# Kernel tuning notes

Hardware: AMD Instinct MI355X
Metric: run time of the kernel (lower is better)

## Reference

```python
import jax, jax.numpy as jnp
import numpy as np

BS, NQ, DIM, HEADS, POINTS, LEVELS = 2, 4096, 768, 6, 4, 1
HD = DIM // HEADS
H = W = 64
NV = H * W
EPS = 1e-6


def setup_inputs() -> dict:
    key = jax.random.key(0)
    ks = jax.random.split(key, 16)
    s = 0.02  # param init scale
    return {
        "query": jax.random.normal(ks[0], (BS, NQ, DIM), jnp.float32),
        "reference_points": jax.random.uniform(ks[1], (BS, NQ, LEVELS, 2), jnp.float32),
        "feat": jax.random.normal(ks[2], (BS, NV, DIM), jnp.float32),
        "spatial_shapes": np.array([[H, W]], dtype=np.int64),
        "level_start_index": np.array([0], dtype=np.int64),
        "ln_w": jnp.ones((DIM,), jnp.float32),
        "ln_b": jnp.zeros((DIM,), jnp.float32),
        "vp_w": jax.random.normal(ks[3], (DIM, DIM), jnp.float32) * s,
        "vp_b": jnp.zeros((DIM,), jnp.float32),
        "off_w": jax.random.normal(ks[4], (DIM, HEADS * LEVELS * POINTS * 2), jnp.float32) * s,
        "off_b": jax.random.normal(ks[5], (HEADS * LEVELS * POINTS * 2,), jnp.float32),
        "aw_w": jax.random.normal(ks[6], (DIM, HEADS * LEVELS * POINTS), jnp.float32) * s,
        "aw_b": jnp.zeros((HEADS * LEVELS * POINTS,), jnp.float32),
        "out_w": jax.random.normal(ks[7], (DIM, DIM), jnp.float32) * s,
        "out_b": jnp.zeros((DIM,), jnp.float32),
        "gamma": jax.random.normal(ks[8], (DIM,), jnp.float32) * 0.1,
    }


def _layernorm(x, w, b):
    mu = jnp.mean(x, axis=-1, keepdims=True)
    var = jnp.mean(jnp.square(x - mu), axis=-1, keepdims=True)
    return (x - mu) * jax.lax.rsqrt(var + EPS) * w + b


def _bilinear_sample(img, loc):
    # img: (bs, heads, H, W, hd); loc: (bs, nq, heads, points, 2) in [0,1]
    # matches torch.grid_sample(align_corners=False, padding_mode='zeros')
    bs, heads, h, w, hd = img.shape
    x = loc[..., 0] * w - 0.5
    y = loc[..., 1] * h - 0.5
    x0 = jnp.floor(x)
    y0 = jnp.floor(y)
    wx = x - x0
    wy = y - y0
    x0i = x0.astype(jnp.int32)
    y0i = y0.astype(jnp.int32)
    bi = jnp.arange(bs)[:, None, None, None]
    hi = jnp.arange(heads)[None, None, :, None]

    def gather(yi, xi):
        valid = (xi >= 0) & (xi < w) & (yi >= 0) & (yi < h)
        v = img[bi, hi, jnp.clip(yi, 0, h - 1), jnp.clip(xi, 0, w - 1)]
        return v * valid[..., None].astype(img.dtype)

    v00 = gather(y0i, x0i)
    v01 = gather(y0i, x0i + 1)
    v10 = gather(y0i + 1, x0i)
    v11 = gather(y0i + 1, x0i + 1)
    wx = wx[..., None]
    wy = wy[..., None]
    return (v00 * (1 - wy) * (1 - wx) + v01 * (1 - wy) * wx
            + v10 * wy * (1 - wx) + v11 * wy * wx)


def _msda(q, value, reference_points, spatial_shapes, off_w, off_b, aw_w, aw_b, out_w, out_b):
    bs, nq, _ = q.shape
    nv = value.shape[1]
    value = value.reshape(bs, nv, HEADS, HD)
    offsets = (q @ off_w + off_b).reshape(bs, nq, HEADS, LEVELS, POINTS, 2)
    aw = jax.nn.softmax(q @ aw_w + aw_b, axis=-1).reshape(bs, nq, HEADS, LEVELS, POINTS)
    # offset_normalizer = [W_l, H_l] per level
    norm = jnp.asarray(np.asarray(spatial_shapes)[:, ::-1], jnp.float32)  # (L, 2)
    loc = reference_points[:, :, None, :, None, :] + offsets / norm[None, None, None, :, None, :]
    # loc: (bs, nq, heads, levels, points, 2)
    out = jnp.zeros((bs, nq, HEADS, HD), jnp.float32)
    start = 0
    for l in range(LEVELS):
        h_l, w_l = int(spatial_shapes[l][0]), int(spatial_shapes[l][1])
        img = value[:, start:start + h_l * w_l].reshape(bs, h_l, w_l, HEADS, HD).transpose(0, 3, 1, 2, 4)
        sampled = _bilinear_sample(img, loc[:, :, :, l])  # (bs, nq, heads, points, hd)
        out = out + jnp.einsum('bnhpd,bnhp->bnhd', sampled, aw[:, :, :, l])
        start += h_l * w_l
    return out.reshape(bs, nq, DIM) @ out_w + out_b


def reference(query, reference_points, feat, spatial_shapes, level_start_index,
              ln_w, ln_b, vp_w, vp_b, off_w, off_b, aw_w, aw_b, out_w, out_b, gamma):
    q = _layernorm(query, ln_w, ln_b)
    value = feat @ vp_w + vp_b
    attn = _msda(q, value, reference_points, spatial_shapes,
                 off_w, off_b, aw_w, aw_b, out_w, out_b)
    # identity = zeros, dropout = 0 -> attn as-is; residual scale by gamma
    return query + gamma * attn
```

## Files before the change

### kernel.cpp

```cpp
#include <hip/hip_runtime.h>
#include <hip/hip_bf16.h>
#include <math.h>

#define BSZ 2
#define NQ 4096
#define DIM 768
#define HEADS 6
#define POINTS 4
#define HD 128
#define HW_DIM 64
#define NV (HW_DIM*HW_DIM)
#define M_TOTAL (BSZ*NQ)
#define KDIM 768
#define KSPLIT 2
#define KPART (KDIM/KSPLIT)

#define BM 64
#define BN 128
#define BKK 64
#define NBLK_M (M_TOTAL/BM)
#define NBLK_N (DIM/BN)
#define GEMM_GRID (NBLK_M*NBLK_N)
#define LN_BLOCKS (M_TOTAL/4)
#define TR_BLOCKS (576+576+72)

#define A_TILE (BM*BKK)
#define B_TILE (BN*BKK)
#define SMEM_U16 (2*(A_TILE+B_TILE))

typedef __attribute__((ext_vector_type(8))) short bf16x8;
typedef __attribute__((ext_vector_type(4))) float f32x4;
typedef unsigned int u32;
typedef unsigned short u16;

__device__ inline u16 f2bf(float f) {
    union { float f; u32 u; } v; v.f = f;
    u32 r = v.u + 0x7fffu + ((v.u >> 16) & 1u);
    return (u16)(r >> 16);
}

#define GLD16(g, l) __builtin_amdgcn_global_load_lds( \
    (const __attribute__((address_space(1))) u32*)(g), \
    (__attribute__((address_space(3))) u32*)(l), 16, 0, 0)

__global__ __launch_bounds__(256) void prep_kernel(
        const float* __restrict__ x, const float* __restrict__ lnw,
        const float* __restrict__ lnb, u16* __restrict__ q,
        const float* __restrict__ feat, u16* __restrict__ feat_bf,
        const float* __restrict__ vp_w,  u16* __restrict__ vp_wt,
        const float* __restrict__ out_w, u16* __restrict__ out_wt,
        const float* __restrict__ off_w, const float* __restrict__ aw_w,
        u16* __restrict__ oaw_wt) {
    int b = blockIdx.x;
    if (b < LN_BLOCKS) {
        int wave = threadIdx.x >> 6, lane = threadIdx.x & 63;
        int row = b * 4 + wave;
        int c = lane * 4;
        const float* xr = x + (size_t)row * DIM;
        const float* fr = feat + (size_t)row * DIM;
        float4 v0 = *(const float4*)(xr + c);
        float4 v1 = *(const float4*)(xr + c + 256);
        float4 v2 = *(const float4*)(xr + c + 512);
        float4 f0 = *(const float4*)(fr + c);
        float4 f1 = *(const float4*)(fr + c + 256);
        float4 f2 = *(const float4*)(fr + c + 512);
        u16* fb = feat_bf + (size_t)row * DIM;
        ushort4 fo;
        fo.x = f2bf(f0.x); fo.y = f2bf(f0.y); fo.z = f2bf(f0.z); fo.w = f2bf(f0.w);
        *(ushort4*)(fb + c) = fo;
        fo.x = f2bf(f1.x); fo.y = f2bf(f1.y); fo.z = f2bf(f1.z); fo.w = f2bf(f1.w);
        *(ushort4*)(fb + c + 256) = fo;
        fo.x = f2bf(f2.x); fo.y = f2bf(f2.y); fo.z = f2bf(f2.z); fo.w = f2bf(f2.w);
        *(ushort4*)(fb + c + 512) = fo;

        float s  = v0.x+v0.y+v0.z+v0.w + v1.x+v1.y+v1.z+v1.w + v2.x+v2.y+v2.z+v2.w;
        float ss = v0.x*v0.x+v0.y*v0.y+v0.z*v0.z+v0.w*v0.w
                 + v1.x*v1.x+v1.y*v1.y+v1.z*v1.z+v1.w*v1.w
                 + v2.x*v2.x+v2.y*v2.y+v2.z*v2.z+v2.w*v2.w;
        #pragma unroll
        for (int st = 1; st < 64; st <<= 1) {
            s  += __shfl_xor(s,  st, 64);
            ss += __shfl_xor(ss, st, 64);
        }
        float mean = s * (1.0f / DIM);
        float var  = ss * (1.0f / DIM) - mean * mean;
        float rstd = rsqrtf(var + 1e-6f);
        u16* qr = q + (size_t)row * DIM;
        #pragma unroll
        for (int g = 0; g < 3; g++) {
            float4 v = (g == 0) ? v0 : (g == 1) ? v1 : v2;
            int cc = c + g * 256;
            const float4 ww = *(const float4*)(lnw + cc);
            const float4 bb = *(const float4*)(lnb + cc);
            ushort4 o;
            o.x = f2bf((v.x - mean) * rstd * ww.x + bb.x);
            o.y = f2bf((v.y - mean) * rstd * ww.y + bb.y);
            o.z = f2bf((v.z - mean) * rstd * ww.z + bb.z);
            o.w = f2bf((v.w - mean) * rstd * ww.w + bb.w);
            *(ushort4*)(qr + cc) = o;
        }
    } else {
        int t = b - LN_BLOCKS;
        int z, xk, yk;
        if (t < 576)      { z = 0; xk = t % 24; yk = t / 24; }
        else if (t < 1152){ z = 1; t -= 576; xk = t % 24; yk = t / 24; }
        else              { z = 2; t -= 1152; xk = t % 3; yk = t / 3; }
        __shared__ float tile[32][33];
        int n0 = xk * 32, k0 = yk * 32;
        int tx = threadIdx.x & 31, ty = threadIdx.x >> 5;
        const float* src = (z == 0) ? vp_w : (z == 1) ? out_w : nullptr;
        u16* dst = (z == 0) ? vp_wt : (z == 1) ? out_wt : oaw_wt;
        #pragma unroll
        for (int r = 0; r < 4; r++) {
            int k = k0 + ty + r * 8, n = n0 + tx;
            float v = 0.0f;
            if (z < 2) {
                v = src[(size_t)k * DIM + n];
            } else {
                if (n < 48) v = off_w[(size_t)k * 48 + n];
                else if (n < 72) v = aw_w[(size_t)k * 24 + (n - 48)];
            }
            tile[ty + r * 8][tx] = v;
        }
        __syncthreads();
        #pragma unroll
        for (int r = 0; r < 4; r++) {
            int nn = ty + r * 8, kk = tx;
            int drow = n0 + nn;
            if (z == 2 && drow >= 80) continue;
            dst[(size_t)drow * KDIM + k0 + kk] = f2bf(tile[kk][nn]);
        }
    }
}

__device__ __forceinline__ void gemm_big_body(int b, u16* __restrict__ smem,
        const u16* __restrict__ A, const u16* __restrict__ Bt,
        const float* __restrict__ bias, void* __restrict__ Cout,
        int storeBF16, const float* __restrict__ resid,
        const float* __restrict__ gamma) {
    u16* As = smem;
    u16* Bs = smem + 2 * A_TILE;
    int tid = threadIdx.x, w = tid >> 6, lane = tid & 63;
    int lm = lane & 15, quad = lane >> 4;
    int xcd = b & 7, idx = b >> 3;
    int mb = xcd * 16 + idx / NBLK_N;
    int nb = idx % NBLK_N;
    int m0 = mb * BM, n0 = nb * BN;
    int wr = w & 1, wc = w >> 1;

    int srow = lane >> 3;
    int scol = (lane & 7) ^ srow;
    const u16* Ab = A + (size_t)m0 * KDIM;
    const u16* Bb = Bt + (size_t)n0 * KDIM;

    f32x4 acc[2][4];
    #pragma unroll
    for (int i = 0; i < 2; i++)
        #pragma unroll
        for (int j = 0; j < 4; j++) acc[i][j] = (f32x4){0.f, 0.f, 0.f, 0.f};

    int aoff[2][2], boff[4][2];
    #pragma unroll
    for (int i = 0; i < 2; i++) {
        int row = wr * 32 + i * 16 + lm;
        #pragma unroll
        for (int kk = 0; kk < 2; kk++)
            aoff[i][kk] = row * BKK + (((quad + 4 * kk) ^ (row & 7)) << 3);
    }
    #pragma unroll
    for (int j = 0; j < 4; j++) {
        int row = wc * 64 + j * 16 + lm;
        #pragma unroll
        for (int kk = 0; kk < 2; kk++)
            boff[j][kk] = row * BKK + (((quad + 4 * kk) ^ (row & 7)) << 3);
    }

    auto stage = [&](int buf, int k0) {
        #pragma unroll
        for (int r = 0; r < 2; r++) {
            int row = r * 32 + w * 8 + srow;
            GLD16(Ab + (size_t)row * KDIM + k0 + scol * 8,
                  As + buf * A_TILE + (r * 32 + w * 8) * BKK);
        }
        #pragma unroll
        for (int r = 0; r < 4; r++) {
            int row = r * 32 + w * 8 + srow;
            GLD16(Bb + (size_t)row * KDIM + k0 + scol * 8,
                  Bs + buf * B_TILE + (r * 32 + w * 8) * BKK);
        }
    };

    stage(0, 0);
    __syncthreads();
    const int NT = KDIM / BKK;
    for (int t = 0; t < NT; t++) {
        if (t + 1 < NT) stage((t + 1) & 1, (t + 1) * BKK);
        const u16* Ap = As + (t & 1) * A_TILE;
        const u16* Bp = Bs + (t & 1) * B_TILE;
        #pragma unroll
        for (int kk = 0; kk < 2; kk++) {
            bf16x8 af[2], bf[4];
            #pragma unroll
            for (int i = 0; i < 2; i++) af[i] = *(const bf16x8*)(Ap + aoff[i][kk]);
            #pragma unroll
            for (int j = 0; j < 4; j++) bf[j] = *(const bf16x8*)(Bp + boff[j][kk]);
            #pragma unroll
            for (int i = 0; i < 2; i++)
                #pragma unroll
                for (int j = 0; j < 4; j++)
                    acc[i][j] = __builtin_amdgcn_mfma_f32_16x16x32_bf16(af[i], bf[j], acc[i][j], 0, 0, 0);
        }
        __syncthreads();
    }

    #pragma unroll
    for (int j = 0; j < 4; j++) {
        int col = n0 + wc * 64 + j * 16 + lm;
        float bb = bias[col];
        #pragma unroll
        for (int i = 0; i < 2; i++) {
            #pragma unroll
            for (int r = 0; r < 4; r++) {
                int row = m0 + wr * 32 + i * 16 + quad * 4 + r;
                size_t idxo = (size_t)row * DIM + col;
                float v = acc[i][j][r] + bb;
                if (storeBF16) {
                    ((u16*)Cout)[idxo] = f2bf(v);
                } else {
                    ((float*)Cout)[idxo] = resid[idxo] + gamma[col] * v;
                }
            }
        }
    }
}

#define SA_TILE (64*32)
#define SB_TILE (80*32)
__device__ __forceinline__ void gemm_small_body(int mblk, int part,
        u16* __restrict__ smem,
        const u16* __restrict__ A, const u16* __restrict__ Bt,
        const float* __restrict__ b0, const float* __restrict__ b1,
        float* __restrict__ C) {
    u16* As2 = smem;
    u16* Bs2 = smem + 2 * SA_TILE;
    int tid = threadIdx.x, wave = tid >> 6, lane = tid & 63;
    int lm = lane & 15, quad = lane >> 4;
    int m0 = mblk * 64;
    int kbase = part * KPART;
    f32x4 acc[5];
    #pragma unroll
    for (int i = 0; i < 5; i++) acc[i] = (f32x4){0.f, 0.f, 0.f, 0.f};
    int lrow = lane >> 2, lcol = (lane & 3) * 8;

    auto stage = [&](int buf, int k0) {
        for (int c = wave; c < 9; c += 4) {
            if (c < 4) {
                GLD16(A + (size_t)(m0 + c * 16 + lrow) * KDIM + k0 + lcol,
                      As2 + buf * SA_TILE + c * 16 * 32);
            } else {
                GLD16(Bt + (size_t)((c - 4) * 16 + lrow) * KDIM + k0 + lcol,
                      Bs2 + buf * SB_TILE + (c - 4) * 16 * 32);
            }
        }
    };

    stage(0, kbase);
    __syncthreads();
    const int NT = KPART / 32;
    for (int t = 0; t < NT; t++) {
        if (t + 1 < NT) stage((t + 1) & 1, kbase + (t + 1) * 32);
        const u16* Ap = As2 + (t & 1) * SA_TILE;
        const u16* Bp = Bs2 + (t & 1) * SB_TILE;
        bf16x8 af = *(const bf16x8*)(Ap + (wave * 16 + lm) * 32 + quad * 8);
        #pragma unroll
        for (int bn = 0; bn < 5; bn++) {
            bf16x8 bv = *(const bf16x8*)(Bp + (bn * 16 + lm) * 32 + quad * 8);
            acc[bn] = __builtin_amdgcn_mfma_f32_16x16x32_bf16(af, bv, acc[bn], 0, 0, 0);
        }
        __syncthreads();
    }
    float* Cp = C + (size_t)part * M_TOTAL * 80;
    #pragma unroll
    for (int bn = 0; bn < 5; bn++) {
        int col = bn * 16 + lm;
        float bb = 0.0f;
        if (part == 0) bb = (col < 48) ? b0[col] : ((col < 72) ? b1[col - 48] : 0.0f);
        #pragma unroll
        for (int r = 0; r < 4; r++) {
            int row = m0 + wave * 16 + quad * 4 + r;
            Cp[(size_t)row * 80 + col] = acc[bn][r] + bb;
        }
    }
}

__global__ __launch_bounds__(256, 3) void gemms_kernel(
        const u16* __restrict__ feat_bf, const u16* __restrict__ vp_wt,
        const float* __restrict__ vp_b, u16* __restrict__ v_bf,
        const u16* __restrict__ q_bf, const u16* __restrict__ oaw_wt,
        const float* __restrict__ off_b, const float* __restrict__ aw_b,
        float* __restrict__ oa) {
    __shared__ u16 smem[SMEM_U16];
    int b = blockIdx.x;
    if (b < GEMM_GRID) {
        gemm_big_body(b, smem, feat_bf, vp_wt, vp_b, v_bf, 1, nullptr, nullptr);
    } else {
        int t = b - GEMM_GRID;
        gemm_small_body(t & 127, t >> 7, smem, q_bf, oaw_wt, off_b, aw_b, oa);
    }
}

__global__ __launch_bounds__(256, 3) void outgemm_kernel(
        const u16* __restrict__ s_bf, const u16* __restrict__ out_wt,
        const float* __restrict__ out_b, float* __restrict__ out_f,
        const float* __restrict__ query, const float* __restrict__ gamma) {
    __shared__ u16 smem[SMEM_U16];
    gemm_big_body(blockIdx.x, smem, s_bf, out_wt, out_b, out_f, 0, query, gamma);
}

__global__ __launch_bounds__(192) void sample_kernel(
        const float* __restrict__ oa, const float* __restrict__ refp,
        const u16* __restrict__ v, u16* __restrict__ out) {
    int row = blockIdx.x;
    int b = row >> 12;
    int tid = threadIdx.x;
    __shared__ float s_w[4][24];
    __shared__ int   s_o[4][24];
    __shared__ float s_e[24];
    if (tid < 24) {
        int h = tid >> 2, p = tid & 3;
        float ox = 0.f, oy = 0.f, lg = 0.f;
        #pragma unroll
        for (int part = 0; part < KSPLIT; part++) {
            const float* pp = oa + (size_t)part * M_TOTAL * 80 + (size_t)row * 80;
            ox += pp[h * 8 + p * 2 + 0];
            oy += pp[h * 8 + p * 2 + 1];
            lg += pp[48 + tid];
        }
        float rx = refp[row * 2 + 0], ry = refp[row * 2 + 1];
        float x = (rx + ox * (1.0f / HW_DIM)) * HW_DIM - 0.5f;
        float y = (ry + oy * (1.0f / HW_DIM)) * HW_DIM - 0.5f;
        float fx = floorf(x), fy = floorf(y);
        int x0 = (int)fx, y0 = (int)fy;
        int x1 = x0 + 1, y1 = y0 + 1;
        float wx = x - fx, wy = y - fy;
        float vx0 = (x0 >= 0 && x0 < HW_DIM) ? 1.f : 0.f;
        float vx1 = (x1 >= 0 && x1 < HW_DIM) ? 1.f : 0.f;
        float vy0 = (y0 >= 0 && y0 < HW_DIM) ? 1.f : 0.f;
        float vy1 = (y1 >= 0 && y1 < HW_DIM) ? 1.f : 0.f;
        int xc0 = min(max(x0, 0), HW_DIM - 1), xc1 = min(max(x1, 0), HW_DIM - 1);
        int yc0 = min(max(y0, 0), HW_DIM - 1), yc1 = min(max(y1, 0), HW_DIM - 1);
        int base = b * NV * DIM;
        s_o[0][tid] = base + (yc0 * HW_DIM + xc0) * DIM;
        s_o[1][tid] = base + (yc0 * HW_DIM + xc1) * DIM;
        s_o[2][tid] = base + (yc1 * HW_DIM + xc0) * DIM;
        s_o[3][tid] = base + (yc1 * HW_DIM + xc1) * DIM;
        s_w[0][tid] = (1.f - wy) * (1.f - wx) * vy0 * vx0;
        s_w[1][tid] = (1.f - wy) * wx * vy0 * vx1;
        s_w[2][tid] = wy * (1.f - wx) * vy1 * vx0;
        s_w[3][tid] = wy * wx * vy1 * vx1;
        s_e[tid] = lg;
        float m = s_e[0];
        #pragma unroll
        for (int i = 1; i < 24; i++) m = fmaxf(m, s_e[i]);
        s_e[tid] = expf(lg - m);
    }
    __syncthreads();
    float ssum = 0.0f;
    #pragma unroll
    for (int i = 0; i < 24; i++) ssum += s_e[i];
    float inv = 1.0f / ssum;

    int h = tid >> 5;
    int d4 = (tid & 31) * 4;
    const u16* vb = v + h * HD + d4;
    float a0 = 0.f, a1 = 0.f, a2 = 0.f, a3 = 0.f;
    #pragma unroll
    for (int p = 0; p < 4; p++) {
        int idx = h * 4 + p;
        float aw = s_e[idx] * inv;
        #pragma unroll
        for (int c = 0; c < 4; c++) {
            uint2 u = *(const uint2*)(vb + s_o[c][idx]);
            float w = aw * s_w[c][idx];
            a0 += w * __uint_as_float(u.x << 16);
            a1 += w * __uint_as_float(u.x & 0xffff0000u);
            a2 += w * __uint_as_float(u.y << 16);
            a3 += w * __uint_as_float(u.y & 0xffff0000u);
        }
    }
    uint2 pack;
    pack.x = (u32)f2bf(a0) | ((u32)f2bf(a1) << 16);
    pack.y = (u32)f2bf(a2) | ((u32)f2bf(a3) << 16);
    *(uint2*)&out[(size_t)row * DIM + h * HD + d4] = pack;
}

extern "C" void kernel_launch(void* const* d_in, const int* in_sizes, int n_in,
                              void* d_out, int out_size, void* d_ws, size_t ws_size,
                              hipStream_t stream) {
    const float* query = (const float*)d_in[0];
    const float* refp  = (const float*)d_in[1];
    const float* feat  = (const float*)d_in[2];
    const float* ln_w  = (const float*)d_in[5];
    const float* ln_b  = (const float*)d_in[6];
    const float* vp_w  = (const float*)d_in[7];
    const float* vp_b  = (const float*)d_in[8];
    const float* off_w = (const float*)d_in[9];
    const float* off_b = (const float*)d_in[10];
    const float* aw_w  = (const float*)d_in[11];
    const float* aw_b  = (const float*)d_in[12];
    const float* out_w = (const float*)d_in[13];
    const float* out_b = (const float*)d_in[14];
    const float* gamma = (const float*)d_in[15];

    const size_t MD = (size_t)M_TOTAL * DIM;
    char* ws = (char*)d_ws;
    u16* q_bf    = (u16*)ws;                 ws += MD * 2;
    u16* feat_bf = (u16*)ws;                 ws += MD * 2;
    u16* v_bf    = (u16*)ws;                 ws += MD * 2;
    u16* s_bf    = (u16*)ws;                 ws += MD * 2;
    u16* vp_wt   = (u16*)ws;                 ws += (size_t)DIM * DIM * 2;
    u16* out_wt  = (u16*)ws;                 ws += (size_t)DIM * DIM * 2;
    u16* oaw_wt  = (u16*)ws;                 ws += (size_t)80 * KDIM * 2;
    float* oa    = (float*)ws;               ws += (size_t)KSPLIT * M_TOTAL * 80 * 4;
    float* out_f = (float*)d_out;

    prep_kernel<<<LN_BLOCKS + TR_BLOCKS, 256, 0, stream>>>(
        query, ln_w, ln_b, q_bf, feat, feat_bf,
        vp_w, vp_wt, out_w, out_wt, off_w, aw_w, oaw_wt);
    gemms_kernel<<<GEMM_GRID + 128 * KSPLIT, 256, 0, stream>>>(
        feat_bf, vp_wt, vp_b, v_bf, q_bf, oaw_wt, off_b, aw_b, oa);
    sample_kernel<<<M_TOTAL, 192, 0, stream>>>(oa, refp, v_bf, s_bf);
    outgemm_kernel<<<GEMM_GRID, 256, 0, stream>>>(s_bf, out_wt, out_b, out_f, query, gamma);
}
```

Measured before the change: 176.9 us.

## Fuse softmax and bilinear coefficient precompute into small GEMM; remap sampling grid

```diff
diff --git a/kernel.cpp b/kernel.cpp
--- a/kernel.cpp
+++ b/kernel.cpp
@@ -12,8 +12,6 @@
 #define NV (HW_DIM*HW_DIM)
 #define M_TOTAL (BSZ*NQ)
 #define KDIM 768
-#define KSPLIT 2
-#define KPART (KDIM/KSPLIT)
 
 #define BM 64
 #define BN 128
@@ -23,6 +21,7 @@
 #define GEMM_GRID (NBLK_M*NBLK_N)
 #define LN_BLOCKS (M_TOTAL/4)
 #define TR_BLOCKS (576+576+72)
+#define SMALL_BLOCKS (M_TOTAL/64)
 
 #define A_TILE (BM*BKK)
 #define B_TILE (BN*BKK)
@@ -236,17 +235,17 @@
 
 #define SA_TILE (64*32)
 #define SB_TILE (80*32)
-__device__ __forceinline__ void gemm_small_body(int mblk, int part,
+__device__ __forceinline__ void gemm_small_body(int mblk,
         u16* __restrict__ smem,
         const u16* __restrict__ A, const u16* __restrict__ Bt,
         const float* __restrict__ b0, const float* __restrict__ b1,
-        float* __restrict__ C) {
+        const float* __restrict__ refp,
+        int4* __restrict__ pk_o, float4* __restrict__ pk_w) {
     u16* As2 = smem;
     u16* Bs2 = smem + 2 * SA_TILE;
     int tid = threadIdx.x, wave = tid >> 6, lane = tid & 63;
     int lm = lane & 15, quad = lane >> 4;
     int m0 = mblk * 64;
-    int kbase = part * KPART;
     f32x4 acc[5];
     #pragma unroll
     for (int i = 0; i < 5; i++) acc[i] = (f32x4){0.f, 0.f, 0.f, 0.f};
@@ -264,11 +263,11 @@
         }
     };
 
-    stage(0, kbase);
+    stage(0, 0);
     __syncthreads();
-    const int NT = KPART / 32;
+    const int NT = KDIM / 32;
     for (int t = 0; t < NT; t++) {
-        if (t + 1 < NT) stage((t + 1) & 1, kbase + (t + 1) * 32);
+        if (t + 1 < NT) stage((t + 1) & 1, (t + 1) * 32);
         const u16* Ap = As2 + (t & 1) * SA_TILE;
         const u16* Bp = Bs2 + (t & 1) * SB_TILE;
         bf16x8 af = *(const bf16x8*)(Ap + (wave * 16 + lm) * 32 + quad * 8);
@@ -279,64 +278,42 @@
         }
         __syncthreads();
     }
-    float* Cp = C + (size_t)part * M_TOTAL * 80;
+
+    float* Cs = (float*)smem;
+    float* rowm  = Cs + 64 * 80;
+    float* rowiv = rowm + 64;
     #pragma unroll
     for (int bn = 0; bn < 5; bn++) {
         int col = bn * 16 + lm;
-        float bb = 0.0f;
-        if (part == 0) bb = (col < 48) ? b0[col] : ((col < 72) ? b1[col - 48] : 0.0f);
+        float bb = (col < 48) ? b0[col] : ((col < 72) ? b1[col - 48] : 0.0f);
         #pragma unroll
         for (int r = 0; r < 4; r++) {
-            int row = m0 + wave * 16 + quad * 4 + r;
-            Cp[(size_t)row * 80 + col] = acc[bn][r] + bb;
-        }
-    }
-}
-
-__global__ __launch_bounds__(256, 3) void gemms_kernel(
-        const u16* __restrict__ feat_bf, const u16* __restrict__ vp_wt,
-        const float* __restrict__ vp_b, u16* __restrict__ v_bf,
-        const u16* __restrict__ q_bf, const u16* __restrict__ oaw_wt,
-        const float* __restrict__ off_b, const float* __restrict__ aw_b,
-        float* __restrict__ oa) {
-    __shared__ u16 smem[SMEM_U16];
-    int b = blockIdx.x;
-    if (b < GEMM_GRID) {
-        gemm_big_body(b, smem, feat_bf, vp_wt, vp_b, v_bf, 1, nullptr, nullptr);
-    } else {
-        int t = b - GEMM_GRID;
-        gemm_small_body(t & 127, t >> 7, smem, q_bf, oaw_wt, off_b, aw_b, oa);
-    }
-}
-
-__global__ __launch_bounds__(256, 3) void outgemm_kernel(
-        const u16* __restrict__ s_bf, const u16* __restrict__ out_wt,
-        const float* __restrict__ out_b, float* __restrict__ out_f,
-        const float* __restrict__ query, const float* __restrict__ gamma) {
-    __shared__ u16 smem[SMEM_U16];
-    gemm_big_body(blockIdx.x, smem, s_bf, out_wt, out_b, out_f, 0, query, gamma);
-}
-
-__global__ __launch_bounds__(192) void sample_kernel(
-        const float* __restrict__ oa, const float* __restrict__ refp,
-        const u16* __restrict__ v, u16* __restrict__ out) {
-    int row = blockIdx.x;
-    int b = row >> 12;
-    int tid = threadIdx.x;
-    __shared__ float s_w[4][24];
-    __shared__ int   s_o[4][24];
-    __shared__ float s_e[24];
-    if (tid < 24) {
-        int h = tid >> 2, p = tid & 3;
-        float ox = 0.f, oy = 0.f, lg = 0.f;
-        #pragma unroll
-        for (int part = 0; part < KSPLIT; part++) {
-            const float* pp = oa + (size_t)part * M_TOTAL * 80 + (size_t)row * 80;
-            ox += pp[h * 8 + p * 2 + 0];
-            oy += pp[h * 8 + p * 2 + 1];
-            lg += pp[48 + tid];
-        }
-        float rx = refp[row * 2 + 0], ry = refp[row * 2 + 1];
+            int rl = wave * 16 + quad * 4 + r;
+            Cs[rl * 80 + col] = acc[bn][r] + bb;
+        }
+    }
+    __syncthreads();
+    if (tid < 64) {
+        const float* cr = Cs + tid * 80 + 48;
+        float m = cr[0];
+        #pragma unroll
+        for (int i = 1; i < 24; i++) m = fmaxf(m, cr[i]);
+        float s = 0.f;
+        #pragma unroll
+        for (int i = 0; i < 24; i++) s += expf(cr[i] - m);
+        rowm[tid] = m;
+        rowiv[tid] = 1.0f / s;
+    }
+    __syncthreads();
+    for (int j = tid; j < 64 * 24; j += 256) {
+        int rl = j / 24, idx = j - rl * 24;
+        int h = idx >> 2, p = idx & 3;
+        const float* cr = Cs + rl * 80;
+        float ox = cr[h * 8 + p * 2 + 0];
+        float oy = cr[h * 8 + p * 2 + 1];
+        float aw = expf(cr[48 + idx] - rowm[rl]) * rowiv[rl];
+        int grow = m0 + rl;
+        float rx = refp[grow * 2 + 0], ry = refp[grow * 2 + 1];
         float x = (rx + ox * (1.0f / HW_DIM)) * HW_DIM - 0.5f;
         float y = (ry + oy * (1.0f / HW_DIM)) * HW_DIM - 0.5f;
         float fx = floorf(x), fy = floorf(y);
@@ -349,49 +326,98 @@
         float vy1 = (y1 >= 0 && y1 < HW_DIM) ? 1.f : 0.f;
         int xc0 = min(max(x0, 0), HW_DIM - 1), xc1 = min(max(x1, 0), HW_DIM - 1);
         int yc0 = min(max(y0, 0), HW_DIM - 1), yc1 = min(max(y1, 0), HW_DIM - 1);
-        int base = b * NV * DIM;
-        s_o[0][tid] = base + (yc0 * HW_DIM + xc0) * DIM;
-        s_o[1][tid] = base + (yc0 * HW_DIM + xc1) * DIM;
-        s_o[2][tid] = base + (yc1 * HW_DIM + xc0) * DIM;
-        s_o[3][tid] = base + (yc1 * HW_DIM + xc1) * DIM;
-        s_w[0][tid] = (1.f - wy) * (1.f - wx) * vy0 * vx0;
-        s_w[1][tid] = (1.f - wy) * wx * vy0 * vx1;
-        s_w[2][tid] = wy * (1.f - wx) * vy1 * vx0;
-        s_w[3][tid] = wy * wx * vy1 * vx1;
-        s_e[tid] = lg;
-        float m = s_e[0];
-        #pragma unroll
-        for (int i = 1; i < 24; i++) m = fmaxf(m, s_e[i]);
-        s_e[tid] = expf(lg - m);
+        int base = (grow >> 12) * NV * DIM;
+        int4 o;
+        o.x = base + (yc0 * HW_DIM + xc0) * DIM;
+        o.y = base + (yc0 * HW_DIM + xc1) * DIM;
+        o.z = base + (yc1 * HW_DIM + xc0) * DIM;
+        o.w = base + (yc1 * HW_DIM + xc1) * DIM;
+        float4 wv;
+        wv.x = aw * (1.f - wy) * (1.f - wx) * vy0 * vx0;
+        wv.y = aw * (1.f - wy) * wx * vy0 * vx1;
+        wv.z = aw * wy * (1.f - wx) * vy1 * vx0;
+        wv.w = aw * wy * wx * vy1 * vx1;
+        pk_o[(size_t)grow * 24 + idx] = o;
+        pk_w[(size_t)grow * 24 + idx] = wv;
+    }
+}
+
+__global__ __launch_bounds__(256, 3) void gemms_kernel(
+        const u16* __restrict__ feat_bf, const u16* __restrict__ vp_wt,
+        const float* __restrict__ vp_b, u16* __restrict__ v_bf,
+        const u16* __restrict__ q_bf, const u16* __restrict__ oaw_wt,
+        const float* __restrict__ off_b, const float* __restrict__ aw_b,
+        const float* __restrict__ refp,
+        int4* __restrict__ pk_o, float4* __restrict__ pk_w) {
+    __shared__ __align__(16) u16 smem[SMEM_U16];
+    int b = blockIdx.x;
+    if (b < GEMM_GRID) {
+        gemm_big_body(b, smem, feat_bf, vp_wt, vp_b, v_bf, 1, nullptr, nullptr);
+    } else {
+        gemm_small_body(b - GEMM_GRID, smem, q_bf, oaw_wt, off_b, aw_b,
+                        refp, pk_o, pk_w);
+    }
+}
+
+__global__ __launch_bounds__(256, 3) void outgemm_kernel(
+        const u16* __restrict__ s_bf, const u16* __restrict__ out_wt,
+        const float* __restrict__ out_b, float* __restrict__ out_f,
+        const float* __restrict__ query, const float* __restrict__ gamma) {
+    __shared__ __align__(16) u16 smem[SMEM_U16];
+    gemm_big_body(blockIdx.x, smem, s_bf, out_wt, out_b, out_f, 0, query, gamma);
+}
+
+#define SMP_QPB 16
+#define SMP_COMBOS 24
+#define SMP_BLOCKS (SMP_COMBOS * (NQ / SMP_QPB))
+
+__global__ __launch_bounds__(256) void sample_kernel(
+        const int4* __restrict__ pk_o, const float4* __restrict__ pk_w,
+        const u16* __restrict__ v, u16* __restrict__ out) {
+    int combo = blockIdx.x % SMP_COMBOS;
+    int qblk  = blockIdx.x / SMP_COMBOS;
+    int head  = combo % 6;
+    int rest  = combo / 6;
+    int batch = rest >> 1;
+    int half  = rest & 1;
+    int tid  = threadIdx.x;
+    int q    = tid >> 4;
+    int lane = tid & 15;
+    int row  = batch * NQ + qblk * SMP_QPB + q;
+
+    __shared__ int4   s_o[SMP_QPB][4];
+    __shared__ float4 s_w[SMP_QPB][4];
+    if (lane < 4) {
+        size_t pidx = (size_t)row * 24 + head * 4 + lane;
+        s_o[q][lane] = pk_o[pidx];
+        s_w[q][lane] = pk_w[pidx];
     }
     __syncthreads();
-    float ssum = 0.0f;
-    #pragma unroll
-    for (int i = 0; i < 24; i++) ssum += s_e[i];
-    float inv = 1.0f / ssum;
-
-    int h = tid >> 5;
-    int d4 = (tid & 31) * 4;
-    const u16* vb = v + h * HD + d4;
+
+    int dbase = head * HD + half * 64 + lane * 4;
+    const u16* vb = v + dbase;
     float a0 = 0.f, a1 = 0.f, a2 = 0.f, a3 = 0.f;
     #pragma unroll
     for (int p = 0; p < 4; p++) {
-        int idx = h * 4 + p;
-        float aw = s_e[idx] * inv;
-        #pragma unroll
-        for (int c = 0; c < 4; c++) {
-            uint2 u = *(const uint2*)(vb + s_o[c][idx]);
-            float w = aw * s_w[c][idx];
-            a0 += w * __uint_as_float(u.x << 16);
-            a1 += w * __uint_as_float(u.x & 0xffff0000u);
-            a2 += w * __uint_as_float(u.y << 16);
-            a3 += w * __uint_as_float(u.y & 0xffff0000u);
-        }
+        int4 o = s_o[q][p];
+        float4 wv = s_w[q][p];
+        uint2 u0 = *(const uint2*)(vb + o.x);
+        uint2 u1 = *(const uint2*)(vb + o.y);
+        uint2 u2 = *(const uint2*)(vb + o.z);
+        uint2 u3 = *(const uint2*)(vb + o.w);
+        a0 += wv.x * __uint_as_float(u0.x << 16) + wv.y * __uint_as_float(u1.x << 16)
+            + wv.z * __uint_as_float(u2.x << 16) + wv.w * __uint_as_float(u3.x << 16);
+        a1 += wv.x * __uint_as_float(u0.x & 0xffff0000u) + wv.y * __uint_as_float(u1.x & 0xffff0000u)
+            + wv.z * __uint_as_float(u2.x & 0xffff0000u) + wv.w * __uint_as_float(u3.x & 0xffff0000u);
+        a2 += wv.x * __uint_as_float(u0.y << 16) + wv.y * __uint_as_float(u1.y << 16)
+            + wv.z * __uint_as_float(u2.y << 16) + wv.w * __uint_as_float(u3.y << 16);
+        a3 += wv.x * __uint_as_float(u0.y & 0xffff0000u) + wv.y * __uint_as_float(u1.y & 0xffff0000u)
+            + wv.z * __uint_as_float(u2.y & 0xffff0000u) + wv.w * __uint_as_float(u3.y & 0xffff0000u);
     }
     uint2 pack;
     pack.x = (u32)f2bf(a0) | ((u32)f2bf(a1) << 16);
     pack.y = (u32)f2bf(a2) | ((u32)f2bf(a3) << 16);
-    *(uint2*)&out[(size_t)row * DIM + h * HD + d4] = pack;
+    *(uint2*)&out[(size_t)row * DIM + dbase] = pack;
 }
 
 extern "C" void kernel_launch(void* const* d_in, const int* in_sizes, int n_in,
@@ -421,14 +447,16 @@
     u16* vp_wt   = (u16*)ws;                 ws += (size_t)DIM * DIM * 2;
     u16* out_wt  = (u16*)ws;                 ws += (size_t)DIM * DIM * 2;
     u16* oaw_wt  = (u16*)ws;                 ws += (size_t)80 * KDIM * 2;
-    float* oa    = (float*)ws;               ws += (size_t)KSPLIT * M_TOTAL * 80 * 4;
+    int4* pk_o   = (int4*)ws;                ws += (size_t)M_TOTAL * 24 * 16;
+    float4* pk_w = (float4*)ws;              ws += (size_t)M_TOTAL * 24 * 16;
     float* out_f = (float*)d_out;
 
     prep_kernel<<<LN_BLOCKS + TR_BLOCKS, 256, 0, stream>>>(
         query, ln_w, ln_b, q_bf, feat, feat_bf,
         vp_w, vp_wt, out_w, out_wt, off_w, aw_w, oaw_wt);
-    gemms_kernel<<<GEMM_GRID + 128 * KSPLIT, 256, 0, stream>>>(
-        feat_bf, vp_wt, vp_b, v_bf, q_bf, oaw_wt, off_b, aw_b, oa);
-    sample_kernel<<<M_TOTAL, 192, 0, stream>>>(oa, refp, v_bf, s_bf);
+    gemms_kernel<<<GEMM_GRID + SMALL_BLOCKS, 256, 0, stream>>>(
+        feat_bf, vp_wt, vp_b, v_bf, q_bf, oaw_wt, off_b, aw_b,
+        refp, pk_o, pk_w);
+    sample_kernel<<<SMP_BLOCKS, 256, 0, stream>>>(pk_o, pk_w, v_bf, s_bf);
     outgemm_kernel<<<GEMM_GRID, 256, 0, stream>>>(s_bf, out_wt, out_b, out_f, query, gamma);
 }
```

New measurement: 186.9 us. 1.06x slower.
